# Performance work log

Hardware: AMD Instinct MI355X
Metric: run time of the kernel (lower is better)

Reference implementation:

```python
import jax, jax.numpy as jnp
import numpy as np
from jax import lax

N_EXPERTS = 256
N_GROUP = 8
TOPK_GROUP = 4
TOP_K = 8
AUX_ALPHA = 0.001


def setup_inputs() -> dict:
    key = jax.random.key(0)
    k1, k2 = jax.random.split(key)
    hidden_states = jax.random.normal(k1, (16384, 2048), dtype=jnp.float32)
    weight = jax.random.normal(k2, (N_EXPERTS, 2048), dtype=jnp.float32) * 0.02
    return {"hidden_states": hidden_states, "weight": weight}


def reference(hidden_states, weight):
    n_tokens = hidden_states.shape[0]
    group_size = N_EXPERTS // N_GROUP  # 32

    # gating logits: [N, E]
    logits = jnp.einsum('nh,eh->ne', hidden_states, weight)

    # group-restricted top-k: [N, G, group_size] -> top TOPK_GROUP per group
    group_logits = logits.reshape(n_tokens, N_GROUP, group_size)
    gw, gi = lax.top_k(group_logits, TOPK_GROUP)          # [N, G, tg]
    gw = gw.reshape(n_tokens, N_GROUP * TOPK_GROUP)
    gi = gi.reshape(n_tokens, N_GROUP * TOPK_GROUP)

    # global top-k over the pooled group winners
    topk_weights, ti = lax.top_k(gw, TOP_K)               # [N, K]
    selected_group = ti // TOPK_GROUP
    expert_in_group = jnp.take_along_axis(gi, ti, axis=1)
    topk_idx = selected_group * group_size + expert_in_group  # [N, K]

    # norm_topk_prob=True
    topk_weights = topk_weights / (jnp.sum(topk_weights, axis=-1, keepdims=True) + 1e-20)

    # auxiliary load-balancing loss (training path)
    expert_mask = jax.nn.one_hot(topk_idx.reshape(-1), N_EXPERTS, dtype=jnp.float32)
    expert_counts = expert_mask.mean(axis=0)              # [E]
    expert_probs = jax.nn.softmax(logits, axis=-1).mean(axis=0)  # [E]
    aux_loss = jnp.sum(expert_counts * expert_probs) * AUX_ALPHA

    return topk_idx, topk_weights, aux_loss
```

## Files before the change

kernel.cpp:

```cpp
#include <hip/hip_runtime.h>
#include <math.h>

#define NTOK 16384
#define KD   2048
#define NE   256
#define NCHUNK 128
#define CHUNK_DW 4096
#define TM 16
#define SL 257

__global__ __launch_bounds__(256) void transform_kernel(
    const float* __restrict__ wgt, float* __restrict__ Bt)
{
    const int c  = blockIdx.x >> 2;
    const int qt = blockIdx.x & 3;
    const int o  = qt * 1024 + threadIdx.x * 4;
    const int e  = o >> 4;
    const int l  = ((o & 15) >> 2) ^ ((e >> 1) & 3);
    const float* src = wgt + (size_t)e * KD + 16 * c + l;
    float4 v = make_float4(src[0], src[4], src[8], src[12]);
    *(float4*)(Bt + (size_t)c * CHUNK_DW + o) = v;
}

typedef __attribute__((address_space(1))) const void GV;
typedef __attribute__((address_space(3))) void LV;
__device__ __forceinline__ void gld_lds16(const float* g, float* l) {
    __builtin_amdgcn_global_load_lds((GV*)g, (LV*)l, 16, 0, 0);
}

__global__ __launch_bounds__(256) void gate_kernel(
    const float* __restrict__ hid, const float* __restrict__ Bt,
    float* __restrict__ out, float* __restrict__ cnt, float* __restrict__ prb)
{
    __shared__ union { float bs[2][CHUNK_DW]; float ls[TM][SL]; } sh;
    __shared__ float As[2][TM][16];
    __shared__ float maxS[TM], sumS[TM], invS[TM];

    const int tid  = threadIdx.x;
    const int l    = tid & 3;
    const int eg   = (tid >> 2) & 31;
    const int tg   = tid >> 7;
    const int t0   = blockIdx.x * TM;
    const int lane = tid & 63;
    const int w    = tid >> 6;
    const int swz  = l ^ ((eg >> 1) & 3);

    float acc[8][8];
#pragma unroll
    for (int i = 0; i < 8; ++i)
#pragma unroll
        for (int j = 0; j < 8; ++j) acc[i][j] = 0.f;

    const bool aact = (lane < 16);
    const int  at   = w * 4 + (lane >> 2);
    const int  aq   = lane & 3;
    float av[4];

    auto stageA_load = [&](int c) {
        if (aact)
            *(float4*)av = *(const float4*)(hid + (size_t)(t0 + at) * KD + 16 * c + 4 * aq);
    };
    auto stageA_write = [&](int buf) {
        if (aact) {
#pragma unroll
            for (int ll = 0; ll < 4; ++ll)
                As[buf][at][ll * 4 + aq] = av[ll];
        }
    };
    auto stageB = [&](int c, int buf) {
        const float* src = Bt + (size_t)c * CHUNK_DW + tid * 4;
        float* dst = &sh.bs[buf][tid * 4];
#pragma unroll
        for (int s = 0; s < 4; ++s)
            gld_lds16(src + s * 1024, dst + s * 1024);
    };

    stageA_load(0);
    stageB(0, 0);
    stageA_write(0);
    int cur = 0;

#pragma unroll 1
    for (int c = 0; c < NCHUNK; ++c) {
        __syncthreads();
        const int nxt = cur ^ 1;
        if (c + 1 < NCHUNK) { stageA_load(c + 1); stageB(c + 1, nxt); }

        float4 a[8];
#pragma unroll
        for (int tt = 0; tt < 8; ++tt)
            a[tt] = *(const float4*)&As[cur][tg * 8 + tt][l * 4];
#pragma unroll
        for (int j = 0; j < 8; ++j) {
            const float4 b = *(const float4*)&sh.bs[cur][(eg + 32 * j) * 16 + swz * 4];
#pragma unroll
            for (int tt = 0; tt < 8; ++tt) {
                float s = acc[tt][j];
                s = __fadd_rn(__fmul_rn(a[tt].w, b.w), s);
                s = __fadd_rn(__fmul_rn(a[tt].z, b.z), s);
                s = __fadd_rn(__fmul_rn(a[tt].y, b.y), s);
                s = __fadd_rn(__fmul_rn(a[tt].x, b.x), s);
                acc[tt][j] = s;
            }
        }
        if (c + 1 < NCHUNK) stageA_write(nxt);
        cur = nxt;
    }

    __syncthreads();
#pragma unroll
    for (int tt = 0; tt < 8; ++tt)
#pragma unroll
        for (int j = 0; j < 8; ++j) {
            float s = acc[tt][j];
            s = __fadd_rn(s, __shfl_xor(s, 1));
            s = __fadd_rn(s, __shfl_xor(s, 2));
            if (l == 0) sh.ls[tg * 8 + tt][eg + 32 * j] = s;
        }
    if (tid < TM) sumS[tid] = 0.f;
    __syncthreads();

    if (tid < TM) {
        const float* lr = &sh.ls[tid][0];
        float tv[8]; int ti[8];
#pragma unroll
        for (int j = 0; j < 8; ++j) { tv[j] = -1e30f; ti[j] = 0; }
        float rowmax = -1e30f;

        auto ins8 = [&](float v, int idx) {
#pragma unroll
            for (int p = 0; p < 8; ++p) {
                if (v > tv[p]) {
#pragma unroll
                    for (int q = 7; q > p; --q) { tv[q] = tv[q - 1]; ti[q] = ti[q - 1]; }
                    tv[p] = v; ti[p] = idx;
                    break;
                }
            }
        };

#pragma unroll 1
        for (int g = 0; g < 8; ++g) {
            float v0 = -1e30f, v1 = -1e30f, v2 = -1e30f, v3 = -1e30f;
            int   i0 = 0, i1 = 0, i2 = 0, i3 = 0;
            for (int j = 0; j < 32; ++j) {
                const float v = lr[g * 32 + j];
                if (v > v0)      { v3=v2;i3=i2; v2=v1;i2=i1; v1=v0;i1=i0; v0=v;i0=j; }
                else if (v > v1) { v3=v2;i3=i2; v2=v1;i2=i1; v1=v;i1=j; }
                else if (v > v2) { v3=v2;i3=i2; v2=v;i2=j; }
                else if (v > v3) { v3=v;i3=j; }
            }
            rowmax = fmaxf(rowmax, v0);
            ins8(v0, g * 32 + i0);
            ins8(v1, g * 32 + i1);
            ins8(v2, g * 32 + i2);
            ins8(v3, g * 32 + i3);
        }

        const float s01 = __fadd_rn(tv[0], tv[1]);
        const float s23 = __fadd_rn(tv[2], tv[3]);
        const float s45 = __fadd_rn(tv[4], tv[5]);
        const float s67 = __fadd_rn(tv[6], tv[7]);
        float s = __fadd_rn(__fadd_rn(s01, s23), __fadd_rn(s45, s67));
        s = __fadd_rn(s, 1e-20f);

        const size_t tg2 = (size_t)(t0 + tid);
#pragma unroll
        for (int j = 0; j < 8; ++j) {
            out[tg2 * 8 + j]                    = (float)ti[j];
            out[(size_t)NTOK * 8 + tg2 * 8 + j] = __fdiv_rn(tv[j], s);
            atomicAdd(&cnt[ti[j]], 1.0f);
        }
        maxS[tid] = rowmax;
    }
    __syncthreads();

    {
        const int t  = tid >> 4;
        const int c0 = (tid & 15) * 16;
        const float m = maxS[t];
        float part = 0.f;
#pragma unroll
        for (int j = 0; j < 16; ++j) part += __expf(sh.ls[t][c0 + j] - m);
        atomicAdd(&sumS[t], part);
    }
    __syncthreads();
    if (tid < TM) invS[tid] = 1.0f / sumS[tid];
    __syncthreads();

    {
        float p = 0.f;
#pragma unroll
        for (int n = 0; n < TM; ++n) p += __expf(sh.ls[n][tid] - maxS[n]) * invS[n];
        atomicAdd(&prb[tid], p);
    }
}

__global__ void aux_kernel(const float* __restrict__ cnt,
                           const float* __restrict__ prb,
                           float* __restrict__ out)
{
    const int tid = threadIdx.x;
    float v = cnt[tid] * prb[tid];
#pragma unroll
    for (int off = 32; off; off >>= 1) v += __shfl_down(v, off, 64);
    __shared__ float ps[4];
    if ((tid & 63) == 0) ps[tid >> 6] = v;
    __syncthreads();
    if (tid == 0) {
        const float tot = ps[0] + ps[1] + ps[2] + ps[3];
        out[(size_t)NTOK * 8 * 2] = tot * (0.001f / (131072.0f * 16384.0f));
    }
}

extern "C" void kernel_launch(void* const* d_in, const int* in_sizes, int n_in,
                              void* d_out, int out_size, void* d_ws, size_t ws_size,
                              hipStream_t stream)
{
    (void)in_sizes; (void)n_in; (void)out_size; (void)ws_size;
    const float* hid = (const float*)d_in[0];
    const float* wgt = (const float*)d_in[1];
    float* out = (float*)d_out;
    float* cnt = (float*)d_ws;
    float* prb = cnt + NE;
    float* Bt  = prb + NE;

    hipMemsetAsync(d_ws, 0, 2 * NE * sizeof(float), stream);
    transform_kernel<<<512, 256, 0, stream>>>(wgt, Bt);
    gate_kernel<<<NTOK / TM, 256, 0, stream>>>(hid, Bt, out, cnt, prb);
    aux_kernel<<<1, 256, 0, stream>>>(cnt, prb, out);
}
```

Before: 545.0 us.

## Use split-bf16 MFMA GEMM with exact fp32 recompute for near-tie tokens

The fp32 FMA gating GEMM becomes a bf16 MFMA GEMM. Both operands are split into hi/lo bf16 parts and three MFMAs per tile approximate fp32 precision. Tokens whose top-k selection has near-ties within an epsilon are flagged, and a second kernel recomputes their logits in exact fp32 and patches indices, weights and counts. This moves the main cost onto matrix cores and keeps the selection correct. The costs are an extra kernel launch, atomics for the flag list, and softmax probabilities that stay at approximate precision.

Result: no change. 554.1 us (+1.7%).

```diff
diff --git a/kernel.cpp b/kernel.cpp
--- a/kernel.cpp
+++ b/kernel.cpp
@@ -4,128 +4,335 @@
 #define NTOK 16384
 #define KD   2048
 #define NE   256
-#define NCHUNK 128
-#define CHUNK_DW 4096
-#define TM 16
-#define SL 257
-
-__global__ __launch_bounds__(256) void transform_kernel(
-    const float* __restrict__ wgt, float* __restrict__ Bt)
+#define BM   64
+#define NSTEP 64
+#define EPS  2.5e-4f
+
+using bf16x8 = __attribute__((ext_vector_type(8))) short;
+using f32x16 = __attribute__((ext_vector_type(16))) float;
+using u16 = unsigned short;
+using u32 = unsigned int;
+
+__device__ __forceinline__ u16 f2bf(float x) {
+    u32 u = __float_as_uint(x);
+    return (u16)((u + 0x7FFFu + ((u >> 16) & 1u)) >> 16);
+}
+__device__ __forceinline__ float bf2f(u16 h) {
+    return __uint_as_float(((u32)h) << 16);
+}
+
+__global__ __launch_bounds__(256) void wsplit_kernel(
+    const float* __restrict__ wgt, u16* __restrict__ Whi, u16* __restrict__ Wlo)
 {
-    const int c  = blockIdx.x >> 2;
-    const int qt = blockIdx.x & 3;
-    const int o  = qt * 1024 + threadIdx.x * 4;
-    const int e  = o >> 4;
-    const int l  = ((o & 15) >> 2) ^ ((e >> 1) & 3);
-    const float* src = wgt + (size_t)e * KD + 16 * c + l;
-    float4 v = make_float4(src[0], src[4], src[8], src[12]);
-    *(float4*)(Bt + (size_t)c * CHUNK_DW + o) = v;
-}
-
-typedef __attribute__((address_space(1))) const void GV;
-typedef __attribute__((address_space(3))) void LV;
-__device__ __forceinline__ void gld_lds16(const float* g, float* l) {
-    __builtin_amdgcn_global_load_lds((GV*)g, (LV*)l, 16, 0, 0);
+    const int idx = blockIdx.x * 256 + threadIdx.x;
+    const int e = idx >> 11, k = idx & 2047;
+    const int c = k >> 5, kk = k & 31;
+    const float w = wgt[idx];
+    const u16 hi = f2bf(w);
+    const u16 lo = f2bf(w - bf2f(hi));
+    const int off = c * 8192 + e * 32 + kk;
+    Whi[off] = hi; Wlo[off] = lo;
 }
 
 __global__ __launch_bounds__(256) void gate_kernel(
-    const float* __restrict__ hid, const float* __restrict__ Bt,
-    float* __restrict__ out, float* __restrict__ cnt, float* __restrict__ prb)
+    const float* __restrict__ hid, const u16* __restrict__ Whi, const u16* __restrict__ Wlo,
+    float* __restrict__ out, float* __restrict__ cnt, float* __restrict__ prb,
+    int* __restrict__ flagcnt, int* __restrict__ flaglist)
 {
-    __shared__ union { float bs[2][CHUNK_DW]; float ls[TM][SL]; } sh;
-    __shared__ float As[2][TM][16];
-    __shared__ float maxS[TM], sumS[TM], invS[TM];
+    __shared__ union {
+        struct {
+            u16 ah[2][64][40];
+            u16 al[2][64][40];
+            u16 bh[2][256][40];
+            u16 bl[2][256][40];
+        } st;
+        float ls[64][257];
+    } sh;
+    __shared__ float maxS[64], sumS[64], invS[64];
 
     const int tid  = threadIdx.x;
-    const int l    = tid & 3;
-    const int eg   = (tid >> 2) & 31;
-    const int tg   = tid >> 7;
-    const int t0   = blockIdx.x * TM;
     const int lane = tid & 63;
-    const int w    = tid >> 6;
-    const int swz  = l ^ ((eg >> 1) & 3);
-
-    float acc[8][8];
-#pragma unroll
-    for (int i = 0; i < 8; ++i)
-#pragma unroll
-        for (int j = 0; j < 8; ++j) acc[i][j] = 0.f;
-
-    const bool aact = (lane < 16);
-    const int  at   = w * 4 + (lane >> 2);
-    const int  aq   = lane & 3;
-    float av[4];
-
-    auto stageA_load = [&](int c) {
-        if (aact)
-            *(float4*)av = *(const float4*)(hid + (size_t)(t0 + at) * KD + 16 * c + 4 * aq);
+    const int wv   = tid >> 6;
+    const int ln31 = lane & 31;
+    const int kh8  = (lane >> 5) * 8;
+    const int t0   = blockIdx.x * BM;
+
+    f32x16 acc[2][2];
+#pragma unroll
+    for (int mf = 0; mf < 2; ++mf)
+#pragma unroll
+        for (int nf = 0; nf < 2; ++nf)
+#pragma unroll
+            for (int r = 0; r < 16; ++r) acc[mf][nf][r] = 0.f;
+
+    float4 arg0, arg1;
+    uint4 brgh[4], brgl[4];
+    const int am  = tid >> 2;
+    const int akq = (tid & 3) * 8;
+
+    auto loadA = [&](int c) {
+        const float* p = hid + (size_t)(t0 + am) * KD + c * 32 + akq;
+        arg0 = *(const float4*)p;
+        arg1 = *(const float4*)(p + 4);
     };
-    auto stageA_write = [&](int buf) {
-        if (aact) {
-#pragma unroll
-            for (int ll = 0; ll < 4; ++ll)
-                As[buf][at][ll * 4 + aq] = av[ll];
+    auto loadB = [&](int c) {
+        const u16* ph = Whi + c * 8192 + tid * 32;
+        const u16* pl = Wlo + c * 8192 + tid * 32;
+#pragma unroll
+        for (int i = 0; i < 4; ++i) {
+            brgh[i] = *(const uint4*)(ph + i * 8);
+            brgl[i] = *(const uint4*)(pl + i * 8);
         }
     };
-    auto stageB = [&](int c, int buf) {
-        const float* src = Bt + (size_t)c * CHUNK_DW + tid * 4;
-        float* dst = &sh.bs[buf][tid * 4];
-#pragma unroll
-        for (int s = 0; s < 4; ++s)
-            gld_lds16(src + s * 1024, dst + s * 1024);
+    auto writeA = [&](int buf) {
+        float f[8] = {arg0.x, arg0.y, arg0.z, arg0.w, arg1.x, arg1.y, arg1.z, arg1.w};
+        u16 hi[8], lo[8];
+#pragma unroll
+        for (int i = 0; i < 8; ++i) {
+            hi[i] = f2bf(f[i]);
+            lo[i] = f2bf(f[i] - bf2f(hi[i]));
+        }
+#pragma unroll
+        for (int i = 0; i < 8; ++i) {
+            sh.st.ah[buf][am][akq + i] = hi[i];
+            sh.st.al[buf][am][akq + i] = lo[i];
+        }
     };
-
-    stageA_load(0);
-    stageB(0, 0);
-    stageA_write(0);
+    auto writeB = [&](int buf) {
+#pragma unroll
+        for (int i = 0; i < 4; ++i) {
+            *(uint4*)&sh.st.bh[buf][tid][i * 8] = brgh[i];
+            *(uint4*)&sh.st.bl[buf][tid][i * 8] = brgl[i];
+        }
+    };
+
+    loadA(0); loadB(0);
+    writeA(0); writeB(0);
     int cur = 0;
 
 #pragma unroll 1
-    for (int c = 0; c < NCHUNK; ++c) {
+    for (int c = 0; c < NSTEP; ++c) {
         __syncthreads();
         const int nxt = cur ^ 1;
-        if (c + 1 < NCHUNK) { stageA_load(c + 1); stageB(c + 1, nxt); }
-
-        float4 a[8];
-#pragma unroll
-        for (int tt = 0; tt < 8; ++tt)
-            a[tt] = *(const float4*)&As[cur][tg * 8 + tt][l * 4];
+        if (c + 1 < NSTEP) { loadA(c + 1); loadB(c + 1); }
+
+#pragma unroll
+        for (int s = 0; s < 2; ++s) {
+            bf16x8 ah[2], al2[2], bh[2], bl2[2];
+#pragma unroll
+            for (int mf = 0; mf < 2; ++mf) {
+                const int r = mf * 32 + ln31;
+                ah[mf]  = *(const bf16x8*)&sh.st.ah[cur][r][s * 16 + kh8];
+                al2[mf] = *(const bf16x8*)&sh.st.al[cur][r][s * 16 + kh8];
+            }
+#pragma unroll
+            for (int nf = 0; nf < 2; ++nf) {
+                const int r = wv * 64 + nf * 32 + ln31;
+                bh[nf]  = *(const bf16x8*)&sh.st.bh[cur][r][s * 16 + kh8];
+                bl2[nf] = *(const bf16x8*)&sh.st.bl[cur][r][s * 16 + kh8];
+            }
+#pragma unroll
+            for (int mf = 0; mf < 2; ++mf)
+#pragma unroll
+                for (int nf = 0; nf < 2; ++nf) {
+                    acc[mf][nf] = __builtin_amdgcn_mfma_f32_32x32x16_bf16(ah[mf],  bh[nf],  acc[mf][nf], 0, 0, 0);
+                    acc[mf][nf] = __builtin_amdgcn_mfma_f32_32x32x16_bf16(ah[mf],  bl2[nf], acc[mf][nf], 0, 0, 0);
+                    acc[mf][nf] = __builtin_amdgcn_mfma_f32_32x32x16_bf16(al2[mf], bh[nf],  acc[mf][nf], 0, 0, 0);
+                }
+        }
+        if (c + 1 < NSTEP) { writeA(nxt); writeB(nxt); }
+        cur = nxt;
+    }
+
+    __syncthreads();
+#pragma unroll
+    for (int mf = 0; mf < 2; ++mf)
+#pragma unroll
+        for (int nf = 0; nf < 2; ++nf) {
+            const int col = wv * 64 + nf * 32 + ln31;
+#pragma unroll
+            for (int r = 0; r < 16; ++r) {
+                const int row = mf * 32 + (r & 3) + 8 * (r >> 2) + 4 * (lane >> 5);
+                sh.ls[row][col] = acc[mf][nf][r];
+            }
+        }
+    if (tid < 64) sumS[tid] = 0.f;
+    __syncthreads();
+
+    if (tid < 64) {
+        const float* lr = &sh.ls[tid][0];
+        float tv[9]; int ti[9];
+#pragma unroll
+        for (int j = 0; j < 9; ++j) { tv[j] = -1e30f; ti[j] = 0; }
+        float gv3[8], gv4[8];
+        float rowmax = -1e30f;
+
+        auto ins9 = [&](float v, int idx) {
+#pragma unroll
+            for (int p = 0; p < 9; ++p) {
+                if (v > tv[p]) {
+#pragma unroll
+                    for (int q = 8; q > p; --q) { tv[q] = tv[q - 1]; ti[q] = ti[q - 1]; }
+                    tv[p] = v; ti[p] = idx;
+                    break;
+                }
+            }
+        };
+
+#pragma unroll 1
+        for (int g = 0; g < 8; ++g) {
+            float v0 = -1e30f, v1 = -1e30f, v2 = -1e30f, v3 = -1e30f, v4 = -1e30f;
+            int   i0 = 0, i1 = 0, i2 = 0, i3 = 0;
+            for (int j = 0; j < 32; ++j) {
+                const float v = lr[g * 32 + j];
+                if (v > v0)      { v4=v3; v3=v2;i3=i2; v2=v1;i2=i1; v1=v0;i1=i0; v0=v;i0=j; }
+                else if (v > v1) { v4=v3; v3=v2;i3=i2; v2=v1;i2=i1; v1=v;i1=j; }
+                else if (v > v2) { v4=v3; v3=v2;i3=i2; v2=v;i2=j; }
+                else if (v > v3) { v4=v3; v3=v;i3=j; }
+                else if (v > v4) { v4=v; }
+            }
+            rowmax = fmaxf(rowmax, v0);
+            gv3[g] = v3; gv4[g] = v4;
+            ins9(v0, g * 32 + i0);
+            ins9(v1, g * 32 + i1);
+            ins9(v2, g * 32 + i2);
+            ins9(v3, g * 32 + i3);
+        }
+
+        bool flag = false;
+#pragma unroll
+        for (int r = 0; r < 8; ++r)
+            if (tv[r] - tv[r + 1] < EPS) flag = true;
+#pragma unroll
+        for (int g = 0; g < 8; ++g)
+            if (gv3[g] - gv4[g] < EPS && gv3[g] > tv[7] - EPS) flag = true;
+
+        const float s01 = __fadd_rn(tv[0], tv[1]);
+        const float s23 = __fadd_rn(tv[2], tv[3]);
+        const float s45 = __fadd_rn(tv[4], tv[5]);
+        const float s67 = __fadd_rn(tv[6], tv[7]);
+        float s = __fadd_rn(__fadd_rn(s01, s23), __fadd_rn(s45, s67));
+        s = __fadd_rn(s, 1e-20f);
+
+        const size_t tg2 = (size_t)(t0 + tid);
 #pragma unroll
         for (int j = 0; j < 8; ++j) {
-            const float4 b = *(const float4*)&sh.bs[cur][(eg + 32 * j) * 16 + swz * 4];
-#pragma unroll
-            for (int tt = 0; tt < 8; ++tt) {
-                float s = acc[tt][j];
-                s = __fadd_rn(__fmul_rn(a[tt].w, b.w), s);
-                s = __fadd_rn(__fmul_rn(a[tt].z, b.z), s);
-                s = __fadd_rn(__fmul_rn(a[tt].y, b.y), s);
-                s = __fadd_rn(__fmul_rn(a[tt].x, b.x), s);
-                acc[tt][j] = s;
-            }
-        }
-        if (c + 1 < NCHUNK) stageA_write(nxt);
-        cur = nxt;
-    }
-
-    __syncthreads();
-#pragma unroll
-    for (int tt = 0; tt < 8; ++tt)
+            out[tg2 * 8 + j]                    = (float)ti[j];
+            out[(size_t)NTOK * 8 + tg2 * 8 + j] = __fdiv_rn(tv[j], s);
+            atomicAdd(&cnt[ti[j]], 1.0f);
+        }
+        if (flag) {
+            const int fi = atomicAdd(flagcnt, 1);
+            flaglist[fi] = t0 + tid;
+        }
+        maxS[tid] = rowmax;
+    }
+    __syncthreads();
+
+    {
+        const int t  = tid & 63;
+        const int c0 = (tid >> 6) * 64;
+        const float m = maxS[t];
+        float part = 0.f;
+#pragma unroll
+        for (int j = 0; j < 64; ++j) part += __expf(sh.ls[t][c0 + j] - m);
+        atomicAdd(&sumS[t], part);
+    }
+    __syncthreads();
+    if (tid < 64) invS[tid] = 1.0f / sumS[tid];
+    __syncthreads();
+
+    {
+        float p = 0.f;
+#pragma unroll
+        for (int n = 0; n < 64; ++n) p += __expf(sh.ls[n][tid] - maxS[n]) * invS[n];
+        atomicAdd(&prb[tid], p);
+    }
+}
+
+__global__ __launch_bounds__(256) void exact_kernel(
+    const float* __restrict__ hid, const float* __restrict__ wgt,
+    float* __restrict__ out, float* __restrict__ cnt,
+    const int* __restrict__ flagcnt, const int* __restrict__ flaglist)
+{
+    const int fn = *flagcnt;
+    const int base = blockIdx.x * 8;
+    if (base >= fn) return;
+    const int nt = min(8, fn - base);
+
+    __shared__ float wch[256 * 17];
+    __shared__ float hch[8 * 17];
+    __shared__ float exls[8][257];
+    __shared__ int tk[8];
+
+    const int tid = threadIdx.x;
+    const int tg  = tid >> 7;
+    const int eg  = (tid >> 2) & 31;
+    const int l   = tid & 3;
+
+    if (tid < 8) tk[tid] = (tid < nt) ? flaglist[base + tid] : flaglist[base];
+    __syncthreads();
+
+    float accq[4][8];
+#pragma unroll
+    for (int i = 0; i < 4; ++i)
+#pragma unroll
+        for (int j = 0; j < 8; ++j) accq[i][j] = 0.f;
+
+#pragma unroll 1
+    for (int c = 0; c < 128; ++c) {
+        __syncthreads();
+        {
+            const float* p = wgt + (size_t)tid * KD + c * 16;
+            float4 w0 = *(const float4*)(p);
+            float4 w1 = *(const float4*)(p + 4);
+            float4 w2 = *(const float4*)(p + 8);
+            float4 w3 = *(const float4*)(p + 12);
+            float* wr = &wch[tid * 17];
+            wr[0]=w0.x; wr[1]=w0.y; wr[2]=w0.z; wr[3]=w0.w;
+            wr[4]=w1.x; wr[5]=w1.y; wr[6]=w1.z; wr[7]=w1.w;
+            wr[8]=w2.x; wr[9]=w2.y; wr[10]=w2.z; wr[11]=w2.w;
+            wr[12]=w3.x; wr[13]=w3.y; wr[14]=w3.z; wr[15]=w3.w;
+        }
+        if (tid < 128) {
+            const int tok = tid >> 4, k = tid & 15;
+            hch[tok * 17 + k] = hid[(size_t)tk[tok] * KD + c * 16 + k];
+        }
+        __syncthreads();
+
+#pragma unroll
+        for (int q = 3; q >= 0; --q) {
+            const int k = 4 * q + l;
+            float hv[4], wv2[8];
+#pragma unroll
+            for (int i = 0; i < 4; ++i) hv[i] = hch[(tg * 4 + i) * 17 + k];
+#pragma unroll
+            for (int j = 0; j < 8; ++j) wv2[j] = wch[(j * 32 + eg) * 17 + k];
+#pragma unroll
+            for (int i = 0; i < 4; ++i)
+#pragma unroll
+                for (int j = 0; j < 8; ++j)
+                    accq[i][j] = __fadd_rn(__fmul_rn(hv[i], wv2[j]), accq[i][j]);
+        }
+    }
+
+    __syncthreads();
+#pragma unroll
+    for (int i = 0; i < 4; ++i)
 #pragma unroll
         for (int j = 0; j < 8; ++j) {
-            float s = acc[tt][j];
-            s = __fadd_rn(s, __shfl_xor(s, 1));
-            s = __fadd_rn(s, __shfl_xor(s, 2));
-            if (l == 0) sh.ls[tg * 8 + tt][eg + 32 * j] = s;
-        }
-    if (tid < TM) sumS[tid] = 0.f;
-    __syncthreads();
-
-    if (tid < TM) {
-        const float* lr = &sh.ls[tid][0];
+            float v = accq[i][j];
+            v = __fadd_rn(v, __shfl_xor(v, 1));
+            v = __fadd_rn(v, __shfl_xor(v, 2));
+            if (l == 0) exls[tg * 4 + i][j * 32 + eg] = v;
+        }
+    __syncthreads();
+
+    if (tid < nt) {
+        const float* lr = &exls[tid][0];
         float tv[8]; int ti[8];
 #pragma unroll
         for (int j = 0; j < 8; ++j) { tv[j] = -1e30f; ti[j] = 0; }
-        float rowmax = -1e30f;
 
         auto ins8 = [&](float v, int idx) {
 #pragma unroll
@@ -150,7 +357,6 @@
                 else if (v > v2) { v3=v2;i3=i2; v2=v;i2=j; }
                 else if (v > v3) { v3=v;i3=j; }
             }
-            rowmax = fmaxf(rowmax, v0);
             ins8(v0, g * 32 + i0);
             ins8(v1, g * 32 + i1);
             ins8(v2, g * 32 + i2);
@@ -164,35 +370,17 @@
         float s = __fadd_rn(__fadd_rn(s01, s23), __fadd_rn(s45, s67));
         s = __fadd_rn(s, 1e-20f);
 
-        const size_t tg2 = (size_t)(t0 + tid);
+        const size_t gt = (size_t)tk[tid];
 #pragma unroll
         for (int j = 0; j < 8; ++j) {
-            out[tg2 * 8 + j]                    = (float)ti[j];
-            out[(size_t)NTOK * 8 + tg2 * 8 + j] = __fdiv_rn(tv[j], s);
-            atomicAdd(&cnt[ti[j]], 1.0f);
-        }
-        maxS[tid] = rowmax;
-    }
-    __syncthreads();
-
-    {
-        const int t  = tid >> 4;
-        const int c0 = (tid & 15) * 16;
-        const float m = maxS[t];
-        float part = 0.f;
-#pragma unroll
-        for (int j = 0; j < 16; ++j) part += __expf(sh.ls[t][c0 + j] - m);
-        atomicAdd(&sumS[t], part);
-    }
-    __syncthreads();
-    if (tid < TM) invS[tid] = 1.0f / sumS[tid];
-    __syncthreads();
-
-    {
-        float p = 0.f;
-#pragma unroll
-        for (int n = 0; n < TM; ++n) p += __expf(sh.ls[n][tid] - maxS[n]) * invS[n];
-        atomicAdd(&prb[tid], p);
+            const int oldi = (int)out[gt * 8 + j];
+            if (oldi != ti[j]) {
+                atomicAdd(&cnt[oldi], -1.0f);
+                atomicAdd(&cnt[ti[j]], 1.0f);
+            }
+            out[gt * 8 + j]                    = (float)ti[j];
+            out[(size_t)NTOK * 8 + gt * 8 + j] = __fdiv_rn(tv[j], s);
+        }
     }
 }
 
@@ -221,12 +409,17 @@
     const float* hid = (const float*)d_in[0];
     const float* wgt = (const float*)d_in[1];
     float* out = (float*)d_out;
-    float* cnt = (float*)d_ws;
-    float* prb = cnt + NE;
-    float* Bt  = prb + NE;
-
-    hipMemsetAsync(d_ws, 0, 2 * NE * sizeof(float), stream);
-    transform_kernel<<<512, 256, 0, stream>>>(wgt, Bt);
-    gate_kernel<<<NTOK / TM, 256, 0, stream>>>(hid, Bt, out, cnt, prb);
+
+    float* cnt      = (float*)d_ws;
+    float* prb      = cnt + NE;
+    int*   flagcnt  = (int*)(prb + NE);
+    int*   flaglist = flagcnt + 64;
+    u16*   Whi      = (u16*)(flaglist + NTOK);
+    u16*   Wlo      = Whi + (size_t)NE * KD;
+
+    hipMemsetAsync(d_ws, 0, (2 * NE + 64) * sizeof(float), stream);
+    wsplit_kernel<<<2048, 256, 0, stream>>>(wgt, Whi, Wlo);
+    gate_kernel<<<NTOK / BM, 256, 0, stream>>>(hid, Whi, Wlo, out, cnt, prb, flagcnt, flaglist);
+    exact_kernel<<<NTOK / 8, 256, 0, stream>>>(hid, wgt, out, cnt, flagcnt, flaglist);
     aux_kernel<<<1, 256, 0, stream>>>(cnt, prb, out);
 }
```
